# Optimization experiments

Hardware: AMD Instinct MI355X
Metric: run time of the kernel (lower is better)

Reference implementation:

```python
import jax, jax.numpy as jnp
import numpy as np

C_IN = 256
A = 2086
H_BOARD, W_BOARD = 10, 9
S = H_BOARD * W_BOARD  # 90
E = 2                  # embed dim after 1x1 conv
NH = 2                 # num attention heads (head_dim = 1)
B = 4096
BN_EPS = 1e-5


def setup_inputs() -> dict:
    key = jax.random.key(0)
    ks = jax.random.split(key, 12)
    inp = {
        "x": jax.random.normal(ks[0], (B, C_IN, H_BOARD, W_BOARD), dtype=jnp.float32),
        # 1x1 conv, no bias: weight [out=2, in=256]
        "conv_w": jax.random.normal(ks[1], (E, C_IN), dtype=jnp.float32) * 0.05,
        # BatchNorm2d(2) params / running stats (inference-mode BN)
        "bn_gamma": jnp.ones((E,), dtype=jnp.float32),
        "bn_beta": jnp.zeros((E,), dtype=jnp.float32),
        "bn_mean": jax.random.normal(ks[2], (E,), dtype=jnp.float32) * 0.1,
        "bn_var": jax.random.uniform(ks[3], (E,), dtype=jnp.float32, minval=0.5, maxval=1.5),
        # MultiheadAttention packed in-proj: [3*E, E], bias [3*E]
        "in_proj_w": jax.random.normal(ks[4], (3 * E, E), dtype=jnp.float32) * 0.5,
        "in_proj_b": jax.random.normal(ks[5], (3 * E,), dtype=jnp.float32) * 0.05,
        "out_proj_w": jax.random.normal(ks[6], (E, E), dtype=jnp.float32) * 0.5,
        "out_proj_b": jax.random.normal(ks[7], (E,), dtype=jnp.float32) * 0.05,
        # Linear(2*90 -> 2086)
        "fc_w": jax.random.normal(ks[8], (A, E * S), dtype=jnp.float32) * 0.05,
        "fc_b": jax.random.normal(ks[9], (A,), dtype=jnp.float32) * 0.05,
    }
    return inp


def reference(x, conv_w, bn_gamma, bn_beta, bn_mean, bn_var,
              in_proj_w, in_proj_b, out_proj_w, out_proj_b, fc_w, fc_b):
    b = x.shape[0]
    # 1x1 conv (bias-free) == channel contraction: [b,256,h,w] -> [b,2,h,w]
    y = jnp.einsum('bchw,oc->bohw', x, conv_w)
    # BatchNorm2d (inference): (y - mean) / sqrt(var + eps) * gamma + beta
    scale = (bn_gamma * jax.lax.rsqrt(bn_var + BN_EPS))[None, :, None, None]
    shift = (bn_beta - bn_mean * bn_gamma * jax.lax.rsqrt(bn_var + BN_EPS))[None, :, None, None]
    y = y * scale + shift
    # [b,2,h,w] -> [b, S, 2]  (seq = board cells, feature = 2 channels)
    xf = y.reshape(b, E, S).transpose(0, 2, 1)
    # packed QKV projection
    qkv = xf @ in_proj_w.T + in_proj_b          # [b,S,3E]
    q, k, v = jnp.split(qkv, 3, axis=-1)        # each [b,S,E]
    hd = E // NH                                 # head_dim = 1
    def split_heads(t):
        return t.reshape(b, S, NH, hd).transpose(0, 2, 1, 3)  # [b,nh,S,hd]
    q, k, v = split_heads(q), split_heads(k), split_heads(v)
    scores = jnp.einsum('bhqd,bhkd->bhqk', q, k) / jnp.sqrt(jnp.float32(hd))
    attn = jax.nn.softmax(scores, axis=-1)      # [b,nh,S,S]
    o = jnp.einsum('bhqk,bhkd->bhqd', attn, v)  # [b,nh,S,hd]
    o = o.transpose(0, 2, 1, 3).reshape(b, S, E)
    o = o @ out_proj_w.T + out_proj_b           # [b,S,E]
    # [b,S,E] -> [b,E,S] -> [b, E*S], matching permute(0,2,1).view(b,-1)
    flat = o.transpose(0, 2, 1).reshape(b, E * S)
    logits = flat @ fc_w.T + fc_b               # [b, 2086]
    return logits
```

## Files before the change

### kernel.cpp

```cpp
#include <hip/hip_runtime.h>

#define C_IN    256
#define S_CELLS 90
#define A_OUT   2086
#define K_FC    180
#define B_BATCH 4096

__global__ __launch_bounds__(256) void front_kernel(
    const float* __restrict__ x,
    const float* __restrict__ conv_w,
    const float* __restrict__ bn_gamma,
    const float* __restrict__ bn_beta,
    const float* __restrict__ bn_mean,
    const float* __restrict__ bn_var,
    const float* __restrict__ ipw,
    const float* __restrict__ ipb,
    const float* __restrict__ opw,
    const float* __restrict__ opb,
    float* __restrict__ flat)
{
    __shared__ float4 kvpack[2][S_CELLS];

    const int half = threadIdx.x >> 7;
    const int s    = threadIdx.x & 127;
    const int b    = blockIdx.x * 2 + half;

    float q0 = 0.f, q1 = 0.f;

    if (s < S_CELLS) {
        const float* xb = x + (size_t)b * (C_IN * S_CELLS) + s;
        float a0 = 0.f, a1 = 0.f;
        #pragma unroll 8
        for (int c = 0; c < C_IN; ++c) {
            float xv = xb[(size_t)c * S_CELLS];
            a0 = fmaf(conv_w[c], xv, a0);
            a1 = fmaf(conv_w[C_IN + c], xv, a1);
        }
        const float sc0 = bn_gamma[0] * rsqrtf(bn_var[0] + 1e-5f);
        const float sc1 = bn_gamma[1] * rsqrtf(bn_var[1] + 1e-5f);
        const float y0 = a0 * sc0 + (bn_beta[0] - bn_mean[0] * sc0);
        const float y1 = a1 * sc1 + (bn_beta[1] - bn_mean[1] * sc1);
        q0 = ipw[0] * y0 + ipw[1] * y1 + ipb[0];
        q1 = ipw[2] * y0 + ipw[3] * y1 + ipb[1];
        const float k0 = ipw[4] * y0 + ipw[5]  * y1 + ipb[2];
        const float k1 = ipw[6] * y0 + ipw[7]  * y1 + ipb[3];
        const float v0 = ipw[8] * y0 + ipw[9]  * y1 + ipb[4];
        const float v1 = ipw[10]* y0 + ipw[11] * y1 + ipb[5];
        kvpack[half][s] = make_float4(k0, v0, k1, v1);
    }
    __syncthreads();
    if (s < S_CELLS) {
        float den0 = 0.f, num0 = 0.f, den1 = 0.f, num1 = 0.f;
        #pragma unroll 3
        for (int j = 0; j < S_CELLS; ++j) {
            const float4 kv = kvpack[half][j];
            const float e0 = __expf(q0 * kv.x);
            const float e1 = __expf(q1 * kv.z);
            den0 += e0; num0 = fmaf(e0, kv.y, num0);
            den1 += e1; num1 = fmaf(e1, kv.w, num1);
        }
        const float o0 = num0 / den0;
        const float o1 = num1 / den1;
        const float r0 = opw[0] * o0 + opw[1] * o1 + opb[0];
        const float r1 = opw[2] * o0 + opw[3] * o1 + opb[1];
        flat[(size_t)b * K_FC + s]           = r0;
        flat[(size_t)b * K_FC + S_CELLS + s] = r1;
    }
}

#define BM 64
#define BN 64
#define BK 60

__global__ __launch_bounds__(256) void fc_kernel(
    const float* __restrict__ Af,
    const float* __restrict__ W,
    const float* __restrict__ bias,
    float* __restrict__ out)
{
    __shared__ float As[BK][BM + 4];
    __shared__ float Bs[BK][BN + 4];

    const int tid = threadIdx.x;
    const int tx  = tid & 15;
    const int ty  = tid >> 4;
    const int bm  = blockIdx.y * BM;
    const int bn  = blockIdx.x * BN;

    float acc[4][4] = {};

    for (int k0 = 0; k0 < K_FC; k0 += BK) {
        for (int q = tid; q < BM * (BK / 4); q += 256) {
            const int m  = q / (BK / 4);
            const int kv = q % (BK / 4);
            const float4 v = *(const float4*)(Af + (size_t)(bm + m) * K_FC + k0 + kv * 4);
            const int kk = kv * 4;
            As[kk + 0][m] = v.x; As[kk + 1][m] = v.y;
            As[kk + 2][m] = v.z; As[kk + 3][m] = v.w;
        }
        for (int q = tid; q < BN * (BK / 4); q += 256) {
            const int n  = q / (BK / 4);
            const int kv = q % (BK / 4);
            const int gn = bn + n;
            float4 v = make_float4(0.f, 0.f, 0.f, 0.f);
            if (gn < A_OUT)
                v = *(const float4*)(W + (size_t)gn * K_FC + k0 + kv * 4);
            const int kk = kv * 4;
            Bs[kk + 0][n] = v.x; Bs[kk + 1][n] = v.y;
            Bs[kk + 2][n] = v.z; Bs[kk + 3][n] = v.w;
        }
        __syncthreads();

        #pragma unroll 6
        for (int k = 0; k < BK; ++k) {
            float a[4], bb[4];
            #pragma unroll
            for (int i = 0; i < 4; ++i) a[i] = As[k][ty * 4 + i];
            #pragma unroll
            for (int j = 0; j < 4; ++j) bb[j] = Bs[k][tx * 4 + j];
            #pragma unroll
            for (int i = 0; i < 4; ++i)
                #pragma unroll
                for (int j = 0; j < 4; ++j)
                    acc[i][j] = fmaf(a[i], bb[j], acc[i][j]);
        }
        __syncthreads();
    }

    #pragma unroll
    for (int i = 0; i < 4; ++i) {
        const int gm = bm + ty * 4 + i;
        #pragma unroll
        for (int j = 0; j < 4; ++j) {
            const int gn = bn + tx * 4 + j;
            if (gn < A_OUT)
                out[(size_t)gm * A_OUT + gn] = acc[i][j] + bias[gn];
        }
    }
}

extern "C" void kernel_launch(void* const* d_in, const int* in_sizes, int n_in,
                              void* d_out, int out_size, void* d_ws, size_t ws_size,
                              hipStream_t stream) {
    const float* x        = (const float*)d_in[0];
    const float* conv_w   = (const float*)d_in[1];
    const float* bn_gamma = (const float*)d_in[2];
    const float* bn_beta  = (const float*)d_in[3];
    const float* bn_mean  = (const float*)d_in[4];
    const float* bn_var   = (const float*)d_in[5];
    const float* ipw      = (const float*)d_in[6];
    const float* ipb      = (const float*)d_in[7];
    const float* opw      = (const float*)d_in[8];
    const float* opb      = (const float*)d_in[9];
    const float* fc_w     = (const float*)d_in[10];
    const float* fc_b     = (const float*)d_in[11];
    float* out  = (float*)d_out;
    float* flat = (float*)d_ws;

    front_kernel<<<dim3(B_BATCH / 2), 256, 0, stream>>>(
        x, conv_w, bn_gamma, bn_beta, bn_mean, bn_var,
        ipw, ipb, opw, opb, flat);

    fc_kernel<<<dim3((A_OUT + BN - 1) / BN, B_BATCH / BM), 256, 0, stream>>>(
        flat, fc_w, fc_b, out);
}
```

Baseline: 593.7 us.

## Enlarge FC GEMM tiles to 8x8 per thread and pack four batches per front block

The FC GEMM moves from 64x64 tiles with 4x4 micro-tiles to 128x128 tiles with 8x8 register micro-tiles. It reads shared memory with float4 loads and writes output as float2, aiming to cut shared-memory traffic per FMA and improve reuse. The front kernel now handles four batch items per 384-thread block, 96 threads each, instead of two per 256-thread block with 128 each, so fewer threads sit idle. Trade-offs are higher register pressure from the 64 accumulators, and float2 stores at odd row offsets, since A_OUT is 2086, which may be misaligned for 8-byte access.

```diff
diff --git a/kernel.cpp b/kernel.cpp
--- a/kernel.cpp
+++ b/kernel.cpp
@@ -6,7 +6,7 @@
 #define K_FC    180
 #define B_BATCH 4096
 
-__global__ __launch_bounds__(256) void front_kernel(
+__global__ __launch_bounds__(384) void front_kernel(
     const float* __restrict__ x,
     const float* __restrict__ conv_w,
     const float* __restrict__ bn_gamma,
@@ -19,18 +19,18 @@
     const float* __restrict__ opb,
     float* __restrict__ flat)
 {
-    __shared__ float4 kvpack[2][S_CELLS];
+    __shared__ float4 kvpack[4][S_CELLS];
 
-    const int half = threadIdx.x >> 7;
-    const int s    = threadIdx.x & 127;
-    const int b    = blockIdx.x * 2 + half;
+    const int sub = threadIdx.x / 96;
+    const int s   = threadIdx.x % 96;
+    const int b   = blockIdx.x * 4 + sub;
 
     float q0 = 0.f, q1 = 0.f;
 
     if (s < S_CELLS) {
         const float* xb = x + (size_t)b * (C_IN * S_CELLS) + s;
         float a0 = 0.f, a1 = 0.f;
-        #pragma unroll 8
+        #pragma unroll 16
         for (int c = 0; c < C_IN; ++c) {
             float xv = xb[(size_t)c * S_CELLS];
             a0 = fmaf(conv_w[c], xv, a0);
@@ -46,14 +46,14 @@
         const float k1 = ipw[6] * y0 + ipw[7]  * y1 + ipb[3];
         const float v0 = ipw[8] * y0 + ipw[9]  * y1 + ipb[4];
         const float v1 = ipw[10]* y0 + ipw[11] * y1 + ipb[5];
-        kvpack[half][s] = make_float4(k0, v0, k1, v1);
+        kvpack[sub][s] = make_float4(k0, v0, k1, v1);
     }
     __syncthreads();
     if (s < S_CELLS) {
         float den0 = 0.f, num0 = 0.f, den1 = 0.f, num1 = 0.f;
-        #pragma unroll 3
+        #pragma unroll 5
         for (int j = 0; j < S_CELLS; ++j) {
-            const float4 kv = kvpack[half][j];
+            const float4 kv = kvpack[sub][j];
             const float e0 = __expf(q0 * kv.x);
             const float e1 = __expf(q1 * kv.z);
             den0 += e0; num0 = fmaf(e0, kv.y, num0);
@@ -68,9 +68,10 @@
     }
 }
 
-#define BM 64
-#define BN 64
-#define BK 60
+#define BM 128
+#define BN 128
+#define BK 36
+#define KV4 (BK / 4)
 
 __global__ __launch_bounds__(256) void fc_kernel(
     const float* __restrict__ Af,
@@ -78,8 +79,8 @@
     const float* __restrict__ bias,
     float* __restrict__ out)
 {
-    __shared__ float As[BK][BM + 4];
-    __shared__ float Bs[BK][BN + 4];
+    __shared__ __align__(16) float As[BK][BM + 4];
+    __shared__ __align__(16) float Bs[BK][BN + 4];
 
     const int tid = threadIdx.x;
     const int tx  = tid & 15;
@@ -87,20 +88,20 @@
     const int bm  = blockIdx.y * BM;
     const int bn  = blockIdx.x * BN;
 
-    float acc[4][4] = {};
+    float acc[8][8] = {};
 
     for (int k0 = 0; k0 < K_FC; k0 += BK) {
-        for (int q = tid; q < BM * (BK / 4); q += 256) {
-            const int m  = q / (BK / 4);
-            const int kv = q % (BK / 4);
+        for (int q = tid; q < BM * KV4; q += 256) {
+            const int m  = q / KV4;
+            const int kv = q % KV4;
             const float4 v = *(const float4*)(Af + (size_t)(bm + m) * K_FC + k0 + kv * 4);
             const int kk = kv * 4;
             As[kk + 0][m] = v.x; As[kk + 1][m] = v.y;
             As[kk + 2][m] = v.z; As[kk + 3][m] = v.w;
         }
-        for (int q = tid; q < BN * (BK / 4); q += 256) {
-            const int n  = q / (BK / 4);
-            const int kv = q % (BK / 4);
+        for (int q = tid; q < BN * KV4; q += 256) {
+            const int n  = q / KV4;
+            const int kv = q % KV4;
             const int gn = bn + n;
             float4 v = make_float4(0.f, 0.f, 0.f, 0.f);
             if (gn < A_OUT)
@@ -111,30 +112,37 @@
         }
         __syncthreads();
 
-        #pragma unroll 6
+        #pragma unroll 4
         for (int k = 0; k < BK; ++k) {
-            float a[4], bb[4];
+            float a[8], bb[8];
+            const float4 a0 = *(const float4*)&As[k][ty * 8];
+            const float4 a1 = *(const float4*)&As[k][ty * 8 + 4];
+            const float4 b0 = *(const float4*)&Bs[k][tx * 8];
+            const float4 b1 = *(const float4*)&Bs[k][tx * 8 + 4];
+            a[0]=a0.x; a[1]=a0.y; a[2]=a0.z; a[3]=a0.w;
+            a[4]=a1.x; a[5]=a1.y; a[6]=a1.z; a[7]=a1.w;
+            bb[0]=b0.x; bb[1]=b0.y; bb[2]=b0.z; bb[3]=b0.w;
+            bb[4]=b1.x; bb[5]=b1.y; bb[6]=b1.z; bb[7]=b1.w;
             #pragma unroll
-            for (int i = 0; i < 4; ++i) a[i] = As[k][ty * 4 + i];
-            #pragma unroll
-            for (int j = 0; j < 4; ++j) bb[j] = Bs[k][tx * 4 + j];
-            #pragma unroll
-            for (int i = 0; i < 4; ++i)
+            for (int i = 0; i < 8; ++i)
                 #pragma unroll
-                for (int j = 0; j < 4; ++j)
+                for (int j = 0; j < 8; ++j)
                     acc[i][j] = fmaf(a[i], bb[j], acc[i][j]);
         }
         __syncthreads();
     }
 
     #pragma unroll
-    for (int i = 0; i < 4; ++i) {
-        const int gm = bm + ty * 4 + i;
+    for (int i = 0; i < 8; ++i) {
+        const int gm = bm + ty * 8 + i;
         #pragma unroll
-        for (int j = 0; j < 4; ++j) {
-            const int gn = bn + tx * 4 + j;
-            if (gn < A_OUT)
-                out[(size_t)gm * A_OUT + gn] = acc[i][j] + bias[gn];
+        for (int p = 0; p < 4; ++p) {
+            const int gn = bn + tx * 8 + p * 2;
+            if (gn < A_OUT) {
+                float2 v = make_float2(acc[i][p * 2]     + bias[gn],
+                                       acc[i][p * 2 + 1] + bias[gn + 1]);
+                *(float2*)(out + (size_t)gm * A_OUT + gn) = v;
+            }
         }
     }
 }
@@ -157,7 +165,7 @@
     float* out  = (float*)d_out;
     float* flat = (float*)d_ws;
 
-    front_kernel<<<dim3(B_BATCH / 2), 256, 0, stream>>>(
+    front_kernel<<<dim3(B_BATCH / 4), 384, 0, stream>>>(
         x, conv_w, bn_gamma, bn_beta, bn_mean, bn_var,
         ipw, ipb, opw, opb, flat);
 
```

Result: no change. 593.7 us (-0.0%).
